# Performance work log

Hardware: AMD Instinct MI355X
Metric: run time of the kernel (lower is better)

Reference implementation:

```python
import jax, jax.numpy as jnp
import numpy as np

HEADS = 16
DIM_HEAD = 64


def setup_inputs() -> dict:
    key = jax.random.key(0)
    ks = jax.random.split(key, 5)
    b, n, dim = 4, 2048, 1024
    return {
        "x": jax.random.normal(ks[0], (b, n, dim), dtype=jnp.float32),
        "Wq": jax.random.normal(ks[1], (dim, HEADS * DIM_HEAD), dtype=jnp.float32) * (dim ** -0.5),
        "Wkv": jax.random.normal(ks[2], (dim, DIM_HEAD), dtype=jnp.float32) * (dim ** -0.5),
        "null_kv": jax.random.normal(ks[3], (DIM_HEAD,), dtype=jnp.float32),
        "Wout": jax.random.normal(ks[4], (HEADS * DIM_HEAD, dim), dtype=jnp.float32) * ((HEADS * DIM_HEAD) ** -0.5),
    }


def reference(x, Wq, Wkv, null_kv, Wout):
    b, n, dim = x.shape
    scale = DIM_HEAD ** -0.5
    # q: [b, h, n, d], pre-scaled
    q = (x @ Wq).reshape(b, n, HEADS, DIM_HEAD).transpose(0, 2, 1, 3) * scale
    # shared single-head kv: [b, n, d], prepend null token -> [b, n+1, d]
    kv = x @ Wkv
    kv = jnp.concatenate([jnp.broadcast_to(null_kv, (b, 1, DIM_HEAD)), kv], axis=1)
    # sim: [b, h, n, n+1]
    sim = jnp.einsum('bhid,bjd->bhij', q, kv)
    mask_value = -jnp.finfo(sim.dtype).max
    # causal: query i may attend kv cols 0..i+1 (null at col 0)
    i, j = sim.shape[-2], sim.shape[-1]
    causal_mask = jnp.triu(jnp.ones((i, j), dtype=bool), k=j - i + 1)
    sim = jnp.where(causal_mask, mask_value, sim)
    attn = jax.nn.softmax(sim.astype(jnp.float32), axis=-1)
    out = jnp.einsum('bhij,bjd->bhid', attn, kv.astype(jnp.float32))
    out = out.transpose(0, 2, 1, 3).reshape(b, n, HEADS * DIM_HEAD)
    return out @ Wout
```

## Files before the change

kernel.cpp:

```cpp
#include <hip/hip_runtime.h>
#include <hip/hip_bf16.h>

#define HEADS  16
#define DHEAD  64
#define BATCH  4
#define SEQ    2048
#define DIM    1024
#define KVROWS 2112

typedef __hip_bfloat16 bf16;
typedef __attribute__((ext_vector_type(8))) short s8v;
typedef __attribute__((ext_vector_type(4))) short s4v;
typedef __attribute__((ext_vector_type(4))) float f4v;

__global__ void convert_kernel(const float* __restrict__ in, bf16* __restrict__ out) {
  const size_t i = ((size_t)blockIdx.x * 256 + threadIdx.x) * 8;
  const float4 a = *(const float4*)&in[i];
  const float4 b = *(const float4*)&in[i + 4];
  bf16 v[8] = {__float2bfloat16(a.x), __float2bfloat16(a.y),
               __float2bfloat16(a.z), __float2bfloat16(a.w),
               __float2bfloat16(b.x), __float2bfloat16(b.y),
               __float2bfloat16(b.z), __float2bfloat16(b.w)};
  *(s8v*)&out[i] = *(s8v*)v;
}

__global__ void transpose_kernel(const float* __restrict__ in, bf16* __restrict__ out,
                                 int R, int C) {
  __shared__ bf16 tile[32][33];
  const int c0 = blockIdx.x * 32, r0 = blockIdx.y * 32;
  const int tx = threadIdx.x, ty = threadIdx.y;
#pragma unroll
  for (int i = 0; i < 32; i += 8)
    tile[ty + i][tx] = __float2bfloat16(in[(size_t)(r0 + ty + i) * C + c0 + tx]);
  __syncthreads();
#pragma unroll
  for (int i = 0; i < 32; i += 8)
    out[(size_t)(c0 + ty + i) * R + r0 + tx] = tile[tx][ty + i];
}

template <typename OT>
__global__ __launch_bounds__(256) void gemm_bt_kernel(
    const bf16* __restrict__ A, const bf16* __restrict__ BT,
    OT* __restrict__ C, int K, int c_ld, float alpha, int kv_remap) {
  __shared__ bf16 As[128][32];
  __shared__ bf16 Bs[64][32];
  const int m0 = blockIdx.x * 128, n0 = blockIdx.y * 64;
  const int t = threadIdx.x;
  const int w = t >> 6, l = t & 63, lr = l & 15, lq = l >> 4;
  f4v acc[2][4] = {};
  const int arow = t >> 1, acol = (t & 1) * 16;
  const int brow = t >> 2, bcol = (t & 3) * 8;

  for (int k0 = 0; k0 < K; k0 += 32) {
    __syncthreads();
    *(s8v*)&As[arow][acol]     = *(const s8v*)&A[(size_t)(m0 + arow) * K + k0 + acol];
    *(s8v*)&As[arow][acol + 8] = *(const s8v*)&A[(size_t)(m0 + arow) * K + k0 + acol + 8];
    *(s8v*)&Bs[brow][bcol]     = *(const s8v*)&BT[(size_t)(n0 + brow) * K + k0 + bcol];
    __syncthreads();
    s8v a0 = *(const s8v*)&As[w * 32 + lr][lq * 8];
    s8v a1 = *(const s8v*)&As[w * 32 + 16 + lr][lq * 8];
#pragma unroll
    for (int ct = 0; ct < 4; ct++) {
      s8v bf = *(const s8v*)&Bs[ct * 16 + lr][lq * 8];
      acc[0][ct] = __builtin_amdgcn_mfma_f32_16x16x32_bf16(a0, bf, acc[0][ct], 0, 0, 0);
      acc[1][ct] = __builtin_amdgcn_mfma_f32_16x16x32_bf16(a1, bf, acc[1][ct], 0, 0, 0);
    }
  }
#pragma unroll
  for (int mt = 0; mt < 2; mt++)
#pragma unroll
    for (int ct = 0; ct < 4; ct++)
#pragma unroll
      for (int r = 0; r < 4; r++) {
        int row = m0 + w * 32 + mt * 16 + lq * 4 + r;
        const int col = n0 + ct * 16 + lr;
        if (kv_remap) row = (row >> 11) * KVROWS + (row & 2047) + 1;
        const float v = acc[mt][ct][r] * alpha;
        if constexpr (__is_same(OT, float)) C[(size_t)row * c_ld + col] = v;
        else                                C[(size_t)row * c_ld + col] = __float2bfloat16(v);
      }
}

__global__ void fill_null_tail_kernel(const float* __restrict__ null_kv,
                                      bf16* __restrict__ kvbuf) {
  const int idx = blockIdx.x * 256 + threadIdx.x;
  const int d = idx & 63;
  const int s = (idx >> 6) & 63;
  const int b = idx >> 12;
  const int row = (s == 0) ? 0 : 2048 + s;
  kvbuf[(size_t)(b * KVROWS + row) * DHEAD + d] =
      (s == 0) ? __float2bfloat16(null_kv[d]) : __float2bfloat16(0.f);
}

__global__ __launch_bounds__(256) void attn_kernel(
    const bf16* __restrict__ q,
    const bf16* __restrict__ kv,
    bf16* __restrict__ o) {
  __shared__ bf16 kvs [64][72];
  __shared__ bf16 kvsT[64][72];
  __shared__ bf16 Ps[4][16][72];
  const int t = threadIdx.x, w = t >> 6, l = t & 63, lr = l & 15, lq = l >> 4;
  const int blk = blockIdx.x;
  const int qt = 31 - (blk >> 6);
  const int hb = blk & 63, h = hb >> 2, b = hb & 3;
  const int q0 = qt * 64;
  const int iw = q0 + w * 16 + lr;

  const bf16* qrow = q + ((size_t)(b * SEQ) + iw) * DIM + h * DHEAD;
  const s8v qb0 = *(const s8v*)&qrow[lq * 8];
  const s8v qb1 = *(const s8v*)&qrow[32 + lq * 8];

  f4v oaccT[4] = {};
  float m_i = -1e30f, l_i = 0.f;

  const bf16* kvb = kv + (size_t)b * KVROWS * DHEAD;
  const int jend = q0 + 65;
  const int srow = t >> 2, scol = (t & 3) * 16;

  for (int j0 = 0; j0 < jend; j0 += 64) {
    __syncthreads();
    s8v r0 = *(const s8v*)&kvb[(size_t)(j0 + srow) * DHEAD + scol];
    s8v r1 = *(const s8v*)&kvb[(size_t)(j0 + srow) * DHEAD + scol + 8];
    *(s8v*)&kvs[srow][scol]     = r0;
    *(s8v*)&kvs[srow][scol + 8] = r1;
    const short* rr0 = (const short*)&r0;
    const short* rr1 = (const short*)&r1;
#pragma unroll
    for (int i2 = 0; i2 < 8; i2++) {
      ((short*)kvsT)[(scol + i2) * 72 + srow]     = rr0[i2];
      ((short*)kvsT)[(scol + 8 + i2) * 72 + srow] = rr1[i2];
    }
    __syncthreads();

    f4v st[4];
#pragma unroll
    for (int jt = 0; jt < 4; jt++) {
      f4v z = {0.f, 0.f, 0.f, 0.f};
      s8v a0 = *(const s8v*)&kvs[jt * 16 + lr][lq * 8];
      s8v a1 = *(const s8v*)&kvs[jt * 16 + lr][32 + lq * 8];
      z = __builtin_amdgcn_mfma_f32_16x16x32_bf16(a0, qb0, z, 0, 0, 0);
      z = __builtin_amdgcn_mfma_f32_16x16x32_bf16(a1, qb1, z, 0, 0, 0);
      st[jt] = z;
    }

    float mx = -1e30f;
#pragma unroll
    for (int jt = 0; jt < 4; jt++)
#pragma unroll
      for (int r = 0; r < 4; r++) {
        const int jg = j0 + jt * 16 + lq * 4 + r;
        float v = (jg > iw + 1) ? -1e30f : st[jt][r];
        st[jt][r] = v;
        mx = fmaxf(mx, v);
      }
    mx = fmaxf(mx, __shfl_xor(mx, 16));
    mx = fmaxf(mx, __shfl_xor(mx, 32));
    const float mnew = fmaxf(m_i, mx);
    const float alpha = exp2f(m_i - mnew);
    m_i = mnew;
    float rs = 0.f;
#pragma unroll
    for (int jt = 0; jt < 4; jt++)
#pragma unroll
      for (int r = 0; r < 4; r++) {
        const float pv = exp2f(st[jt][r] - mnew);
        st[jt][r] = pv;
        rs += pv;
      }
    rs += __shfl_xor(rs, 16);
    rs += __shfl_xor(rs, 32);
    l_i = l_i * alpha + rs;
#pragma unroll
    for (int dt = 0; dt < 4; dt++)
#pragma unroll
      for (int r = 0; r < 4; r++) oaccT[dt][r] *= alpha;

#pragma unroll
    for (int jt = 0; jt < 4; jt++) {
      s4v pk;
#pragma unroll
      for (int r = 0; r < 4; r++) {
        bf16 h16 = __float2bfloat16(st[jt][r]);
        pk[r] = *(short*)&h16;
      }
      *(s4v*)&Ps[w][lr][jt * 16 + lq * 4] = pk;
    }

    const s8v pb0 = *(const s8v*)&Ps[w][lr][lq * 8];
    const s8v pb1 = *(const s8v*)&Ps[w][lr][32 + lq * 8];
#pragma unroll
    for (int dt = 0; dt < 4; dt++) {
      s8v a0 = *(const s8v*)&kvsT[dt * 16 + lr][lq * 8];
      s8v a1 = *(const s8v*)&kvsT[dt * 16 + lr][32 + lq * 8];
      oaccT[dt] = __builtin_amdgcn_mfma_f32_16x16x32_bf16(a0, pb0, oaccT[dt], 0, 0, 0);
      oaccT[dt] = __builtin_amdgcn_mfma_f32_16x16x32_bf16(a1, pb1, oaccT[dt], 0, 0, 0);
    }
  }

  const float inv = 1.0f / l_i;
#pragma unroll
  for (int dt = 0; dt < 4; dt++) {
    s4v pk;
#pragma unroll
    for (int r = 0; r < 4; r++) {
      bf16 h16 = __float2bfloat16(oaccT[dt][r] * inv);
      pk[r] = *(short*)&h16;
    }
    *(s4v*)&Ps[w][lr][dt * 16 + lq * 4] = pk;
  }
  const int orow = l >> 2, od = (l & 3) * 16;
  s8v o0 = *(const s8v*)&Ps[w][orow][od];
  s8v o1 = *(const s8v*)&Ps[w][orow][od + 8];
  bf16* op = o + ((size_t)(b * SEQ) + q0 + w * 16 + orow) * DIM + h * DHEAD + od;
  *(s8v*)&op[0] = o0;
  *(s8v*)&op[8] = o1;
}

extern "C" void kernel_launch(void* const* d_in, const int* in_sizes, int n_in,
                              void* d_out, int out_size, void* d_ws, size_t ws_size,
                              hipStream_t stream) {
  const float* x       = (const float*)d_in[0];
  const float* Wq      = (const float*)d_in[1];
  const float* Wkv     = (const float*)d_in[2];
  const float* null_kv = (const float*)d_in[3];
  const float* Wout    = (const float*)d_in[4];
  float* out = (float*)d_out;

  bf16* q = (bf16*)d_out;
  char* p = (char*)d_ws;
  bf16* att   = (bf16*)p;
  bf16* xb    = (bf16*)(p + (size_t)16 * 1024 * 1024);
  bf16* WoutT = (bf16*)(p + (size_t)32 * 1024 * 1024);
  bf16* kvbuf = (bf16*)(p + (size_t)34 * 1024 * 1024);
  bf16* WqT   = att;
  bf16* WkvT  = att + (size_t)DIM * DIM;

  convert_kernel<<<(BATCH * SEQ * DIM) / (256 * 8), 256, 0, stream>>>(x, xb);

  const dim3 tb(32, 8);
  transpose_kernel<<<dim3(32, 32), tb, 0, stream>>>(Wq,   WqT,   DIM, DIM);
  transpose_kernel<<<dim3(2, 32),  tb, 0, stream>>>(Wkv,  WkvT,  DIM, DHEAD);
  transpose_kernel<<<dim3(32, 32), tb, 0, stream>>>(Wout, WoutT, DIM, DIM);

  gemm_bt_kernel<bf16><<<dim3(64, 16), 256, 0, stream>>>(xb, WqT, q, DIM, DIM,
                                                         0.125f * 1.44269504089f, 0);
  gemm_bt_kernel<bf16><<<dim3(64, 1), 256, 0, stream>>>(xb, WkvT, kvbuf, DIM, DHEAD, 1.0f, 1);
  fill_null_tail_kernel<<<(BATCH * 64 * 64) / 256, 256, 0, stream>>>(null_kv, kvbuf);
  attn_kernel<<<BATCH * HEADS * (SEQ / 64), 256, 0, stream>>>(q, kvbuf, att);
  gemm_bt_kernel<float><<<dim3(64, 16), 256, 0, stream>>>(att, WoutT, out, DIM, DIM, 1.0f, 0);
}
```

Measured before the change: 279.6 us.

## Enlarge GEMM tiles, precompute transposed KV, and process 128 queries per attention block

Measured after the change: 286.3 us. 2.4% more time.

```diff
diff --git a/kernel.cpp b/kernel.cpp
--- a/kernel.cpp
+++ b/kernel.cpp
@@ -39,12 +39,56 @@
 }
 
 template <typename OT>
-__global__ __launch_bounds__(256) void gemm_bt_kernel(
+__global__ __launch_bounds__(256) void gemm128_kernel(
     const bf16* __restrict__ A, const bf16* __restrict__ BT,
-    OT* __restrict__ C, int K, int c_ld, float alpha, int kv_remap) {
+    OT* __restrict__ C, int K, int c_ld, float alpha) {
+  __shared__ bf16 As[128][36];
+  __shared__ bf16 Bs[128][36];
+  const int m0 = blockIdx.x * 128, n0 = blockIdx.y * 128;
+  const int t = threadIdx.x;
+  const int w = t >> 6, l = t & 63, lr = l & 15, lq = l >> 4;
+  const int wm = (w & 1) * 64, wn = (w >> 1) * 64;
+  f4v acc[4][4] = {};
+  const int srow = t >> 1, scol = (t & 1) * 16;
+
+  for (int k0 = 0; k0 < K; k0 += 32) {
+    __syncthreads();
+    *(s8v*)&As[srow][scol]     = *(const s8v*)&A[(size_t)(m0 + srow) * K + k0 + scol];
+    *(s8v*)&As[srow][scol + 8] = *(const s8v*)&A[(size_t)(m0 + srow) * K + k0 + scol + 8];
+    *(s8v*)&Bs[srow][scol]     = *(const s8v*)&BT[(size_t)(n0 + srow) * K + k0 + scol];
+    *(s8v*)&Bs[srow][scol + 8] = *(const s8v*)&BT[(size_t)(n0 + srow) * K + k0 + scol + 8];
+    __syncthreads();
+    s8v a[4], b[4];
+#pragma unroll
+    for (int mt = 0; mt < 4; mt++) a[mt] = *(const s8v*)&As[wm + mt * 16 + lr][lq * 8];
+#pragma unroll
+    for (int ct = 0; ct < 4; ct++) b[ct] = *(const s8v*)&Bs[wn + ct * 16 + lr][lq * 8];
+#pragma unroll
+    for (int mt = 0; mt < 4; mt++)
+#pragma unroll
+      for (int ct = 0; ct < 4; ct++)
+        acc[mt][ct] = __builtin_amdgcn_mfma_f32_16x16x32_bf16(a[mt], b[ct], acc[mt][ct], 0, 0, 0);
+  }
+#pragma unroll
+  for (int mt = 0; mt < 4; mt++)
+#pragma unroll
+    for (int ct = 0; ct < 4; ct++)
+#pragma unroll
+      for (int r = 0; r < 4; r++) {
+        const int row = m0 + wm + mt * 16 + lq * 4 + r;
+        const int col = n0 + wn + ct * 16 + lr;
+        const float v = acc[mt][ct][r] * alpha;
+        if constexpr (__is_same(OT, float)) C[(size_t)row * c_ld + col] = v;
+        else                                C[(size_t)row * c_ld + col] = __float2bfloat16(v);
+      }
+}
+
+__global__ __launch_bounds__(256) void gemm_kv_kernel(
+    const bf16* __restrict__ A, const bf16* __restrict__ BT,
+    bf16* __restrict__ kvbuf, bf16* __restrict__ kvbufT, int K) {
   __shared__ bf16 As[128][32];
   __shared__ bf16 Bs[64][32];
-  const int m0 = blockIdx.x * 128, n0 = blockIdx.y * 64;
+  const int m0 = blockIdx.x * 128;
   const int t = threadIdx.x;
   const int w = t >> 6, l = t & 63, lr = l & 15, lq = l >> 4;
   f4v acc[2][4] = {};
@@ -55,7 +99,7 @@
     __syncthreads();
     *(s8v*)&As[arow][acol]     = *(const s8v*)&A[(size_t)(m0 + arow) * K + k0 + acol];
     *(s8v*)&As[arow][acol + 8] = *(const s8v*)&A[(size_t)(m0 + arow) * K + k0 + acol + 8];
-    *(s8v*)&Bs[brow][bcol]     = *(const s8v*)&BT[(size_t)(n0 + brow) * K + k0 + bcol];
+    *(s8v*)&Bs[brow][bcol]     = *(const s8v*)&BT[(size_t)brow * K + k0 + bcol];
     __syncthreads();
     s8v a0 = *(const s8v*)&As[w * 32 + lr][lq * 8];
     s8v a1 = *(const s8v*)&As[w * 32 + 16 + lr][lq * 8];
@@ -72,148 +116,168 @@
     for (int ct = 0; ct < 4; ct++)
 #pragma unroll
       for (int r = 0; r < 4; r++) {
-        int row = m0 + w * 32 + mt * 16 + lq * 4 + r;
-        const int col = n0 + ct * 16 + lr;
-        if (kv_remap) row = (row >> 11) * KVROWS + (row & 2047) + 1;
-        const float v = acc[mt][ct][r] * alpha;
-        if constexpr (__is_same(OT, float)) C[(size_t)row * c_ld + col] = v;
-        else                                C[(size_t)row * c_ld + col] = __float2bfloat16(v);
+        const int m = m0 + w * 32 + mt * 16 + lq * 4 + r;
+        const int col = ct * 16 + lr;
+        const int bb = m >> 11, jj = (m & 2047) + 1;
+        const bf16 v = __float2bfloat16(acc[mt][ct][r]);
+        kvbuf [(size_t)(bb * KVROWS + jj) * DHEAD + col] = v;
+        kvbufT[(size_t)(bb * DHEAD + col) * KVROWS + jj] = v;
       }
 }
 
 __global__ void fill_null_tail_kernel(const float* __restrict__ null_kv,
-                                      bf16* __restrict__ kvbuf) {
+                                      bf16* __restrict__ kvbuf,
+                                      bf16* __restrict__ kvbufT) {
   const int idx = blockIdx.x * 256 + threadIdx.x;
   const int d = idx & 63;
   const int s = (idx >> 6) & 63;
   const int b = idx >> 12;
   const int row = (s == 0) ? 0 : 2048 + s;
-  kvbuf[(size_t)(b * KVROWS + row) * DHEAD + d] =
-      (s == 0) ? __float2bfloat16(null_kv[d]) : __float2bfloat16(0.f);
+  const bf16 v = (s == 0) ? __float2bfloat16(null_kv[d]) : __float2bfloat16(0.f);
+  kvbuf [(size_t)(b * KVROWS + row) * DHEAD + d] = v;
+  kvbufT[(size_t)(b * DHEAD + d) * KVROWS + row] = v;
 }
 
 __global__ __launch_bounds__(256) void attn_kernel(
     const bf16* __restrict__ q,
     const bf16* __restrict__ kv,
+    const bf16* __restrict__ kvT,
     bf16* __restrict__ o) {
   __shared__ bf16 kvs [64][72];
   __shared__ bf16 kvsT[64][72];
-  __shared__ bf16 Ps[4][16][72];
+  __shared__ bf16 Ps[4][32][72];
   const int t = threadIdx.x, w = t >> 6, l = t & 63, lr = l & 15, lq = l >> 4;
   const int blk = blockIdx.x;
-  const int qt = 31 - (blk >> 6);
+  const int qt = 15 - (blk >> 6);
   const int hb = blk & 63, h = hb >> 2, b = hb & 3;
-  const int q0 = qt * 64;
-  const int iw = q0 + w * 16 + lr;
-
-  const bf16* qrow = q + ((size_t)(b * SEQ) + iw) * DIM + h * DHEAD;
-  const s8v qb0 = *(const s8v*)&qrow[lq * 8];
-  const s8v qb1 = *(const s8v*)&qrow[32 + lq * 8];
-
-  f4v oaccT[4] = {};
-  float m_i = -1e30f, l_i = 0.f;
-
-  const bf16* kvb = kv + (size_t)b * KVROWS * DHEAD;
-  const int jend = q0 + 65;
+  const int q0 = qt * 128;
+
+  s8v qb[2][2];
+#pragma unroll
+  for (int g = 0; g < 2; g++) {
+    const bf16* qrow = q + ((size_t)(b * SEQ) + q0 + w * 32 + g * 16 + lr) * DIM + h * DHEAD;
+    qb[g][0] = *(const s8v*)&qrow[lq * 8];
+    qb[g][1] = *(const s8v*)&qrow[32 + lq * 8];
+  }
+
+  f4v oaccT[2][4] = {};
+  float m_i[2] = {-1e30f, -1e30f}, l_i[2] = {0.f, 0.f};
+
+  const bf16* kvb  = kv  + (size_t)b * KVROWS * DHEAD;
+  const bf16* kvTb = kvT + (size_t)b * DHEAD * KVROWS;
+  const int jend = q0 + 129;
   const int srow = t >> 2, scol = (t & 3) * 16;
 
   for (int j0 = 0; j0 < jend; j0 += 64) {
     __syncthreads();
-    s8v r0 = *(const s8v*)&kvb[(size_t)(j0 + srow) * DHEAD + scol];
-    s8v r1 = *(const s8v*)&kvb[(size_t)(j0 + srow) * DHEAD + scol + 8];
-    *(s8v*)&kvs[srow][scol]     = r0;
-    *(s8v*)&kvs[srow][scol + 8] = r1;
-    const short* rr0 = (const short*)&r0;
-    const short* rr1 = (const short*)&r1;
-#pragma unroll
-    for (int i2 = 0; i2 < 8; i2++) {
-      ((short*)kvsT)[(scol + i2) * 72 + srow]     = rr0[i2];
-      ((short*)kvsT)[(scol + 8 + i2) * 72 + srow] = rr1[i2];
-    }
-    __syncthreads();
-
-    f4v st[4];
+    *(s8v*)&kvs[srow][scol]      = *(const s8v*)&kvb[(size_t)(j0 + srow) * DHEAD + scol];
+    *(s8v*)&kvs[srow][scol + 8]  = *(const s8v*)&kvb[(size_t)(j0 + srow) * DHEAD + scol + 8];
+    *(s8v*)&kvsT[srow][scol]     = *(const s8v*)&kvTb[(size_t)srow * KVROWS + j0 + scol];
+    *(s8v*)&kvsT[srow][scol + 8] = *(const s8v*)&kvTb[(size_t)srow * KVROWS + j0 + scol + 8];
+    __syncthreads();
+
+    f4v st[2][4];
 #pragma unroll
     for (int jt = 0; jt < 4; jt++) {
-      f4v z = {0.f, 0.f, 0.f, 0.f};
       s8v a0 = *(const s8v*)&kvs[jt * 16 + lr][lq * 8];
       s8v a1 = *(const s8v*)&kvs[jt * 16 + lr][32 + lq * 8];
-      z = __builtin_amdgcn_mfma_f32_16x16x32_bf16(a0, qb0, z, 0, 0, 0);
-      z = __builtin_amdgcn_mfma_f32_16x16x32_bf16(a1, qb1, z, 0, 0, 0);
-      st[jt] = z;
-    }
-
-    float mx = -1e30f;
-#pragma unroll
-    for (int jt = 0; jt < 4; jt++)
-#pragma unroll
-      for (int r = 0; r < 4; r++) {
-        const int jg = j0 + jt * 16 + lq * 4 + r;
-        float v = (jg > iw + 1) ? -1e30f : st[jt][r];
-        st[jt][r] = v;
-        mx = fmaxf(mx, v);
-      }
-    mx = fmaxf(mx, __shfl_xor(mx, 16));
-    mx = fmaxf(mx, __shfl_xor(mx, 32));
-    const float mnew = fmaxf(m_i, mx);
-    const float alpha = exp2f(m_i - mnew);
-    m_i = mnew;
-    float rs = 0.f;
-#pragma unroll
-    for (int jt = 0; jt < 4; jt++)
-#pragma unroll
-      for (int r = 0; r < 4; r++) {
-        const float pv = exp2f(st[jt][r] - mnew);
-        st[jt][r] = pv;
-        rs += pv;
-      }
-    rs += __shfl_xor(rs, 16);
-    rs += __shfl_xor(rs, 32);
-    l_i = l_i * alpha + rs;
-#pragma unroll
-    for (int dt = 0; dt < 4; dt++)
-#pragma unroll
-      for (int r = 0; r < 4; r++) oaccT[dt][r] *= alpha;
-
-#pragma unroll
-    for (int jt = 0; jt < 4; jt++) {
-      s4v pk;
-#pragma unroll
-      for (int r = 0; r < 4; r++) {
-        bf16 h16 = __float2bfloat16(st[jt][r]);
-        pk[r] = *(short*)&h16;
-      }
-      *(s4v*)&Ps[w][lr][jt * 16 + lq * 4] = pk;
-    }
-
-    const s8v pb0 = *(const s8v*)&Ps[w][lr][lq * 8];
-    const s8v pb1 = *(const s8v*)&Ps[w][lr][32 + lq * 8];
+#pragma unroll
+      for (int g = 0; g < 2; g++) {
+        f4v z = {0.f, 0.f, 0.f, 0.f};
+        z = __builtin_amdgcn_mfma_f32_16x16x32_bf16(a0, qb[g][0], z, 0, 0, 0);
+        z = __builtin_amdgcn_mfma_f32_16x16x32_bf16(a1, qb[g][1], z, 0, 0, 0);
+        st[g][jt] = z;
+      }
+    }
+
+#pragma unroll
+    for (int g = 0; g < 2; g++) {
+      const int ig = q0 + w * 32 + g * 16 + lr;
+      float mx = -1e30f;
+#pragma unroll
+      for (int jt = 0; jt < 4; jt++)
+#pragma unroll
+        for (int r = 0; r < 4; r++) {
+          const int jg = j0 + jt * 16 + lq * 4 + r;
+          float v = (jg > ig + 1) ? -1e30f : st[g][jt][r];
+          st[g][jt][r] = v;
+          mx = fmaxf(mx, v);
+        }
+      mx = fmaxf(mx, __shfl_xor(mx, 16));
+      mx = fmaxf(mx, __shfl_xor(mx, 32));
+      const float mnew = fmaxf(m_i[g], mx);
+      const float alpha = exp2f(m_i[g] - mnew);
+      m_i[g] = mnew;
+      float rs = 0.f;
+#pragma unroll
+      for (int jt = 0; jt < 4; jt++)
+#pragma unroll
+        for (int r = 0; r < 4; r++) {
+          const float pv = exp2f(st[g][jt][r] - mnew);
+          st[g][jt][r] = pv;
+          rs += pv;
+        }
+      rs += __shfl_xor(rs, 16);
+      rs += __shfl_xor(rs, 32);
+      l_i[g] = l_i[g] * alpha + rs;
+#pragma unroll
+      for (int dt = 0; dt < 4; dt++)
+#pragma unroll
+        for (int r = 0; r < 4; r++) oaccT[g][dt][r] *= alpha;
+
+#pragma unroll
+      for (int jt = 0; jt < 4; jt++) {
+        s4v pk;
+#pragma unroll
+        for (int r = 0; r < 4; r++) {
+          bf16 h16 = __float2bfloat16(st[g][jt][r]);
+          pk[r] = *(short*)&h16;
+        }
+        *(s4v*)&Ps[w][g * 16 + lr][jt * 16 + lq * 4] = pk;
+      }
+    }
+
+    s8v pb[2][2];
+#pragma unroll
+    for (int g = 0; g < 2; g++) {
+      pb[g][0] = *(const s8v*)&Ps[w][g * 16 + lr][lq * 8];
+      pb[g][1] = *(const s8v*)&Ps[w][g * 16 + lr][32 + lq * 8];
+    }
 #pragma unroll
     for (int dt = 0; dt < 4; dt++) {
       s8v a0 = *(const s8v*)&kvsT[dt * 16 + lr][lq * 8];
       s8v a1 = *(const s8v*)&kvsT[dt * 16 + lr][32 + lq * 8];
-      oaccT[dt] = __builtin_amdgcn_mfma_f32_16x16x32_bf16(a0, pb0, oaccT[dt], 0, 0, 0);
-      oaccT[dt] = __builtin_amdgcn_mfma_f32_16x16x32_bf16(a1, pb1, oaccT[dt], 0, 0, 0);
-    }
-  }
-
-  const float inv = 1.0f / l_i;
-#pragma unroll
-  for (int dt = 0; dt < 4; dt++) {
-    s4v pk;
-#pragma unroll
-    for (int r = 0; r < 4; r++) {
-      bf16 h16 = __float2bfloat16(oaccT[dt][r] * inv);
-      pk[r] = *(short*)&h16;
-    }
-    *(s4v*)&Ps[w][lr][dt * 16 + lq * 4] = pk;
-  }
-  const int orow = l >> 2, od = (l & 3) * 16;
-  s8v o0 = *(const s8v*)&Ps[w][orow][od];
-  s8v o1 = *(const s8v*)&Ps[w][orow][od + 8];
-  bf16* op = o + ((size_t)(b * SEQ) + q0 + w * 16 + orow) * DIM + h * DHEAD + od;
-  *(s8v*)&op[0] = o0;
-  *(s8v*)&op[8] = o1;
+#pragma unroll
+      for (int g = 0; g < 2; g++) {
+        oaccT[g][dt] = __builtin_amdgcn_mfma_f32_16x16x32_bf16(a0, pb[g][0], oaccT[g][dt], 0, 0, 0);
+        oaccT[g][dt] = __builtin_amdgcn_mfma_f32_16x16x32_bf16(a1, pb[g][1], oaccT[g][dt], 0, 0, 0);
+      }
+    }
+  }
+
+#pragma unroll
+  for (int g = 0; g < 2; g++) {
+    const float inv = 1.0f / l_i[g];
+#pragma unroll
+    for (int dt = 0; dt < 4; dt++) {
+      s4v pk;
+#pragma unroll
+      for (int r = 0; r < 4; r++) {
+        bf16 h16 = __float2bfloat16(oaccT[g][dt][r] * inv);
+        pk[r] = *(short*)&h16;
+      }
+      *(s4v*)&Ps[w][g * 16 + lr][dt * 16 + lq * 4] = pk;
+    }
+  }
+#pragma unroll
+  for (int g = 0; g < 2; g++) {
+    const int orow = l >> 2, od = (l & 3) * 16;
+    s8v o0 = *(const s8v*)&Ps[w][g * 16 + orow][od];
+    s8v o1 = *(const s8v*)&Ps[w][g * 16 + orow][od + 8];
+    bf16* op = o + ((size_t)(b * SEQ) + q0 + w * 32 + g * 16 + orow) * DIM + h * DHEAD + od;
+    *(s8v*)&op[0] = o0;
+    *(s8v*)&op[8] = o1;
+  }
 }
 
 extern "C" void kernel_launch(void* const* d_in, const int* in_sizes, int n_in,
@@ -226,7 +290,8 @@
   const float* Wout    = (const float*)d_in[4];
   float* out = (float*)d_out;
 
-  bf16* q = (bf16*)d_out;
+  bf16* q      = (bf16*)d_out;
+  bf16* kvbufT = (bf16*)((char*)d_out + (size_t)16 * 1024 * 1024);
   char* p = (char*)d_ws;
   bf16* att   = (bf16*)p;
   bf16* xb    = (bf16*)(p + (size_t)16 * 1024 * 1024);
@@ -242,10 +307,10 @@
   transpose_kernel<<<dim3(2, 32),  tb, 0, stream>>>(Wkv,  WkvT,  DIM, DHEAD);
   transpose_kernel<<<dim3(32, 32), tb, 0, stream>>>(Wout, WoutT, DIM, DIM);
 
-  gemm_bt_kernel<bf16><<<dim3(64, 16), 256, 0, stream>>>(xb, WqT, q, DIM, DIM,
-                                                         0.125f * 1.44269504089f, 0);
-  gemm_bt_kernel<bf16><<<dim3(64, 1), 256, 0, stream>>>(xb, WkvT, kvbuf, DIM, DHEAD, 1.0f, 1);
-  fill_null_tail_kernel<<<(BATCH * 64 * 64) / 256, 256, 0, stream>>>(null_kv, kvbuf);
-  attn_kernel<<<BATCH * HEADS * (SEQ / 64), 256, 0, stream>>>(q, kvbuf, att);
-  gemm_bt_kernel<float><<<dim3(64, 16), 256, 0, stream>>>(att, WoutT, out, DIM, DIM, 1.0f, 0);
-}
+  gemm128_kernel<bf16><<<dim3(64, 8), 256, 0, stream>>>(xb, WqT, q, DIM, DIM,
+                                                        0.125f * 1.44269504089f);
+  gemm_kv_kernel<<<64, 256, 0, stream>>>(xb, WkvT, kvbuf, kvbufT, DIM);
+  fill_null_tail_kernel<<<(BATCH * 64 * 64) / 256, 256, 0, stream>>>(null_kv, kvbuf, kvbufT);
+  attn_kernel<<<BATCH * HEADS * (SEQ / 128), 256, 0, stream>>>(q, kvbuf, kvbufT, att);
+  gemm128_kernel<float><<<dim3(64, 8), 256, 0, stream>>>(att, WoutT, out, DIM, DIM, 1.0f);
+}
```

## Use async global-to-LDS GEMM, pre-transposed KV buffer, and skip unneeded causal masking

Applied to the files above, without the earlier changes.

New measurement: 257.5 us. -7.9%, faster.

```diff
diff --git a/kernel.cpp b/kernel.cpp
--- a/kernel.cpp
+++ b/kernel.cpp
@@ -12,6 +12,12 @@
 typedef __attribute__((ext_vector_type(8))) short s8v;
 typedef __attribute__((ext_vector_type(4))) short s4v;
 typedef __attribute__((ext_vector_type(4))) float f4v;
+
+__device__ __forceinline__ void gl_lds16(const void* g, void* l) {
+  __builtin_amdgcn_global_load_lds(
+      (const __attribute__((address_space(1))) unsigned int*)g,
+      (__attribute__((address_space(3))) unsigned int*)l, 16, 0, 0);
+}
 
 __global__ void convert_kernel(const float* __restrict__ in, bf16* __restrict__ out) {
   const size_t i = ((size_t)blockIdx.x * 256 + threadIdx.x) * 8;
@@ -39,12 +45,70 @@
 }
 
 template <typename OT>
-__global__ __launch_bounds__(256) void gemm_bt_kernel(
+__global__ __launch_bounds__(256) void gemm_async_kernel(
     const bf16* __restrict__ A, const bf16* __restrict__ BT,
-    OT* __restrict__ C, int K, int c_ld, float alpha, int kv_remap) {
+    OT* __restrict__ C, int K, int c_ld, float alpha) {
+  __shared__ bf16 As[128 * 32];
+  __shared__ bf16 Bs[128 * 32];
+  const int m0 = blockIdx.x * 128, n0 = blockIdx.y * 128;
+  const int t = threadIdx.x;
+  const int w = t >> 6, l = t & 63, lr = l & 15, lq = l >> 4;
+  const int wm = (w & 1) * 64, wn = (w >> 1) * 64;
+  f4v acc[4][4] = {};
+
+  const int rowl = l >> 2;
+  const int cl = ((l & 3) ^ ((l >> 3) & 3)) * 8;
+  const bf16* gA0 = A  + (size_t)(m0 + 32 * w + rowl) * K + cl;
+  const bf16* gA1 = A  + (size_t)(m0 + 32 * w + 16 + rowl) * K + cl;
+  const bf16* gB0 = BT + (size_t)(n0 + 32 * w + rowl) * K + cl;
+  const bf16* gB1 = BT + (size_t)(n0 + 32 * w + 16 + rowl) * K + cl;
+  bf16* lA0 = As + (2 * w) * 512;
+  bf16* lA1 = As + (2 * w + 1) * 512;
+  bf16* lB0 = Bs + (2 * w) * 512;
+  bf16* lB1 = Bs + (2 * w + 1) * 512;
+
+  const int sw = lq ^ ((lr >> 1) & 3);
+  const s8v* As16 = (const s8v*)As;
+  const s8v* Bs16 = (const s8v*)Bs;
+
+  for (int k0 = 0; k0 < K; k0 += 32) {
+    __syncthreads();
+    gl_lds16(gA0 + k0, lA0);
+    gl_lds16(gA1 + k0, lA1);
+    gl_lds16(gB0 + k0, lB0);
+    gl_lds16(gB1 + k0, lB1);
+    __syncthreads();
+    s8v a[4], b[4];
+#pragma unroll
+    for (int mt = 0; mt < 4; mt++) a[mt] = As16[(wm + mt * 16 + lr) * 4 + sw];
+#pragma unroll
+    for (int ct = 0; ct < 4; ct++) b[ct] = Bs16[(wn + ct * 16 + lr) * 4 + sw];
+#pragma unroll
+    for (int mt = 0; mt < 4; mt++)
+#pragma unroll
+      for (int ct = 0; ct < 4; ct++)
+        acc[mt][ct] = __builtin_amdgcn_mfma_f32_16x16x32_bf16(a[mt], b[ct], acc[mt][ct], 0, 0, 0);
+  }
+#pragma unroll
+  for (int mt = 0; mt < 4; mt++)
+#pragma unroll
+    for (int ct = 0; ct < 4; ct++)
+#pragma unroll
+      for (int r = 0; r < 4; r++) {
+        const int row = m0 + wm + mt * 16 + lq * 4 + r;
+        const int col = n0 + wn + ct * 16 + lr;
+        const float v = acc[mt][ct][r] * alpha;
+        if constexpr (__is_same(OT, float)) C[(size_t)row * c_ld + col] = v;
+        else                                C[(size_t)row * c_ld + col] = __float2bfloat16(v);
+      }
+}
+
+__global__ __launch_bounds__(256) void gemm_kv_kernel(
+    const bf16* __restrict__ A, const bf16* __restrict__ BT,
+    bf16* __restrict__ kvbuf, bf16* __restrict__ kvbufT, int K) {
   __shared__ bf16 As[128][32];
   __shared__ bf16 Bs[64][32];
-  const int m0 = blockIdx.x * 128, n0 = blockIdx.y * 64;
+  const int m0 = blockIdx.x * 128;
   const int t = threadIdx.x;
   const int w = t >> 6, l = t & 63, lr = l & 15, lq = l >> 4;
   f4v acc[2][4] = {};
@@ -55,7 +119,7 @@
     __syncthreads();
     *(s8v*)&As[arow][acol]     = *(const s8v*)&A[(size_t)(m0 + arow) * K + k0 + acol];
     *(s8v*)&As[arow][acol + 8] = *(const s8v*)&A[(size_t)(m0 + arow) * K + k0 + acol + 8];
-    *(s8v*)&Bs[brow][bcol]     = *(const s8v*)&BT[(size_t)(n0 + brow) * K + k0 + bcol];
+    *(s8v*)&Bs[brow][bcol]     = *(const s8v*)&BT[(size_t)brow * K + k0 + bcol];
     __syncthreads();
     s8v a0 = *(const s8v*)&As[w * 32 + lr][lq * 8];
     s8v a1 = *(const s8v*)&As[w * 32 + 16 + lr][lq * 8];
@@ -72,29 +136,32 @@
     for (int ct = 0; ct < 4; ct++)
 #pragma unroll
       for (int r = 0; r < 4; r++) {
-        int row = m0 + w * 32 + mt * 16 + lq * 4 + r;
-        const int col = n0 + ct * 16 + lr;
-        if (kv_remap) row = (row >> 11) * KVROWS + (row & 2047) + 1;
-        const float v = acc[mt][ct][r] * alpha;
-        if constexpr (__is_same(OT, float)) C[(size_t)row * c_ld + col] = v;
-        else                                C[(size_t)row * c_ld + col] = __float2bfloat16(v);
+        const int m = m0 + w * 32 + mt * 16 + lq * 4 + r;
+        const int col = ct * 16 + lr;
+        const int bb = m >> 11, jj = (m & 2047) + 1;
+        const bf16 v = __float2bfloat16(acc[mt][ct][r]);
+        kvbuf [(size_t)(bb * KVROWS + jj) * DHEAD + col] = v;
+        kvbufT[(size_t)(bb * DHEAD + col) * KVROWS + jj] = v;
       }
 }
 
 __global__ void fill_null_tail_kernel(const float* __restrict__ null_kv,
-                                      bf16* __restrict__ kvbuf) {
+                                      bf16* __restrict__ kvbuf,
+                                      bf16* __restrict__ kvbufT) {
   const int idx = blockIdx.x * 256 + threadIdx.x;
   const int d = idx & 63;
   const int s = (idx >> 6) & 63;
   const int b = idx >> 12;
   const int row = (s == 0) ? 0 : 2048 + s;
-  kvbuf[(size_t)(b * KVROWS + row) * DHEAD + d] =
-      (s == 0) ? __float2bfloat16(null_kv[d]) : __float2bfloat16(0.f);
+  const bf16 v = (s == 0) ? __float2bfloat16(null_kv[d]) : __float2bfloat16(0.f);
+  kvbuf [(size_t)(b * KVROWS + row) * DHEAD + d] = v;
+  kvbufT[(size_t)(b * DHEAD + d) * KVROWS + row] = v;
 }
 
 __global__ __launch_bounds__(256) void attn_kernel(
     const bf16* __restrict__ q,
     const bf16* __restrict__ kv,
+    const bf16* __restrict__ kvT,
     bf16* __restrict__ o) {
   __shared__ bf16 kvs [64][72];
   __shared__ bf16 kvsT[64][72];
@@ -112,24 +179,17 @@
 
   f4v oaccT[4] = {};
   float m_i = -1e30f, l_i = 0.f;
-
-  const bf16* kvb = kv + (size_t)b * KVROWS * DHEAD;
+  const bf16* kvb  = kv  + (size_t)b * KVROWS * DHEAD;
+  const bf16* kvTb = kvT + (size_t)b * DHEAD * KVROWS;
   const int jend = q0 + 65;
   const int srow = t >> 2, scol = (t & 3) * 16;
 
   for (int j0 = 0; j0 < jend; j0 += 64) {
     __syncthreads();
-    s8v r0 = *(const s8v*)&kvb[(size_t)(j0 + srow) * DHEAD + scol];
-    s8v r1 = *(const s8v*)&kvb[(size_t)(j0 + srow) * DHEAD + scol + 8];
-    *(s8v*)&kvs[srow][scol]     = r0;
-    *(s8v*)&kvs[srow][scol + 8] = r1;
-    const short* rr0 = (const short*)&r0;
-    const short* rr1 = (const short*)&r1;
-#pragma unroll
-    for (int i2 = 0; i2 < 8; i2++) {
-      ((short*)kvsT)[(scol + i2) * 72 + srow]     = rr0[i2];
-      ((short*)kvsT)[(scol + 8 + i2) * 72 + srow] = rr1[i2];
-    }
+    *(s8v*)&kvs[srow][scol]      = *(const s8v*)&kvb[(size_t)(j0 + srow) * DHEAD + scol];
+    *(s8v*)&kvs[srow][scol + 8]  = *(const s8v*)&kvb[(size_t)(j0 + srow) * DHEAD + scol + 8];
+    *(s8v*)&kvsT[srow][scol]     = *(const s8v*)&kvTb[(size_t)srow * KVROWS + j0 + scol];
+    *(s8v*)&kvsT[srow][scol + 8] = *(const s8v*)&kvTb[(size_t)srow * KVROWS + j0 + scol + 8];
     __syncthreads();
 
     f4v st[4];
@@ -144,15 +204,22 @@
     }
 
     float mx = -1e30f;
-#pragma unroll
-    for (int jt = 0; jt < 4; jt++)
-#pragma unroll
-      for (int r = 0; r < 4; r++) {
-        const int jg = j0 + jt * 16 + lq * 4 + r;
-        float v = (jg > iw + 1) ? -1e30f : st[jt][r];
-        st[jt][r] = v;
-        mx = fmaxf(mx, v);
-      }
+    if (j0 + 62 > q0 + w * 16) {
+#pragma unroll
+      for (int jt = 0; jt < 4; jt++)
+#pragma unroll
+        for (int r = 0; r < 4; r++) {
+          const int jg = j0 + jt * 16 + lq * 4 + r;
+          float v = (jg > iw + 1) ? -1e30f : st[jt][r];
+          st[jt][r] = v;
+          mx = fmaxf(mx, v);
+        }
+    } else {
+#pragma unroll
+      for (int jt = 0; jt < 4; jt++)
+#pragma unroll
+        for (int r = 0; r < 4; r++) mx = fmaxf(mx, st[jt][r]);
+    }
     mx = fmaxf(mx, __shfl_xor(mx, 16));
     mx = fmaxf(mx, __shfl_xor(mx, 32));
     const float mnew = fmaxf(m_i, mx);
@@ -226,7 +293,9 @@
   const float* Wout    = (const float*)d_in[4];
   float* out = (float*)d_out;
 
-  bf16* q = (bf16*)d_out;
+  char* dob = (char*)d_out;
+  bf16* q      = (bf16*)dob;
+  bf16* kvbufT = (bf16*)(dob + (size_t)16 * 1024 * 1024);
   char* p = (char*)d_ws;
   bf16* att   = (bf16*)p;
   bf16* xb    = (bf16*)(p + (size_t)16 * 1024 * 1024);
@@ -242,10 +311,12 @@
   transpose_kernel<<<dim3(2, 32),  tb, 0, stream>>>(Wkv,  WkvT,  DIM, DHEAD);
   transpose_kernel<<<dim3(32, 32), tb, 0, stream>>>(Wout, WoutT, DIM, DIM);
 
-  gemm_bt_kernel<bf16><<<dim3(64, 16), 256, 0, stream>>>(xb, WqT, q, DIM, DIM,
-                                                         0.125f * 1.44269504089f, 0);
-  gemm_bt_kernel<bf16><<<dim3(64, 1), 256, 0, stream>>>(xb, WkvT, kvbuf, DIM, DHEAD, 1.0f, 1);
-  fill_null_tail_kernel<<<(BATCH * 64 * 64) / 256, 256, 0, stream>>>(null_kv, kvbuf);
-  attn_kernel<<<BATCH * HEADS * (SEQ / 64), 256, 0, stream>>>(q, kvbuf, att);
-  gemm_bt_kernel<float><<<dim3(64, 16), 256, 0, stream>>>(att, WoutT, out, DIM, DIM, 1.0f, 0);
-}
+  gemm_async_kernel<bf16><<<dim3(64, 8), 256, 0, stream>>>(xb, WqT, q, DIM, DIM,
+                                                           0.125f * 1.44269504089f);
+  gemm_kv_kernel<<<64, 256, 0, stream>>>(xb, WkvT, kvbuf, kvbufT, DIM);
+  fill_null_tail_kernel<<<(BATCH * 64 * 64) / 256, 256, 0, stream>>>(null_kv, kvbuf, kvbufT);
+
+  attn_kernel<<<BATCH * HEADS * (SEQ / 64), 256, 0, stream>>>(q, kvbuf, kvbufT, att);
+
+  gemm_async_kernel<float><<<dim3(64, 8), 256, 0, stream>>>(att, WoutT, out, DIM, DIM, 1.0f);
+}
```
